# Kernel tuning notes

Hardware: AMD Instinct MI355X
Metric: run time of the kernel (lower is better)

Reference implementation:

```python
import math
import jax, jax.numpy as jnp
import numpy as np

BATCH, SEQ, EMBED, HEADS = 2, 2048, 1024, 16
HEAD_DIM = EMBED // HEADS


def setup_inputs() -> dict:
    key = jax.random.key(0)
    k1, k2, k3 = jax.random.split(key, 3)
    scale = 1.0 / math.sqrt(EMBED)  # keep pre-softmax logits in a sane range
    x = jax.random.normal(k1, (BATCH, SEQ, EMBED), dtype=jnp.float32)
    mask = jnp.ones((BATCH, SEQ), dtype=jnp.int32)
    qkv_w = jax.random.normal(k2, (3 * EMBED, EMBED), dtype=jnp.float32) * scale
    out_w = jax.random.normal(k3, (EMBED, EMBED), dtype=jnp.float32) * scale
    out_b = jnp.zeros((EMBED,), dtype=jnp.float32)
    return {"x": x, "mask": mask, "qkv_w": qkv_w, "out_w": out_w, "out_b": out_b}


def reference(x, mask, qkv_w, out_w, out_b):
    b, s, e = x.shape
    # qkv projection (torch Linear: x @ W.T), then split heads
    qkv = (x @ qkv_w.T).reshape(b, s, 3, HEADS, HEAD_DIM)
    q, k, v = qkv[:, :, 0], qkv[:, :, 1], qkv[:, :, 2]  # each [b,s,h,d]
    # full score matrix [b,h,s,s]
    scores = jnp.einsum('bshd,bthd->bhst', q, k) / math.sqrt(HEAD_DIM)
    # mask broadcast over query dim and heads: [b,1,1,s_keys]
    scores = jnp.where(mask[:, None, None, :] == 0, -jnp.inf, scores)
    attn = jax.nn.softmax(scores, axis=-1)
    # dropout is identity in eval mode
    out = jnp.einsum('bhst,bthd->bshd', attn, v).reshape(b, s, e)
    return out @ out_w.T + out_b
```

## Files before the change

kernel.cpp:

```cpp
#include <hip/hip_runtime.h>
#include <hip/hip_bf16.h>

#define BATCH 2
#define SEQ   2048
#define EMBED 1024
#define HEADS 16
#define HDIM  64
#define NBH   (BATCH*HEADS)

typedef __attribute__((ext_vector_type(8))) short short8;
typedef __attribute__((ext_vector_type(4))) float floatx4;
typedef unsigned short u16;
typedef unsigned int   u32;

__device__ __forceinline__ void async_cp16(const void* g, void* l) {
  __builtin_amdgcn_global_load_lds((const __attribute__((address_space(1))) void*)g,
                                   (__attribute__((address_space(3))) void*)l,
                                   16, 0, 0);
}

__device__ __forceinline__ u16 f2b(float f) {
  union { float f; u32 u; } x; x.f = f;
  return (u16)((x.u + 0x7fffu + ((x.u >> 16) & 1u)) >> 16);
}
__device__ __forceinline__ u32 pk2(float a, float b) {
  __hip_bfloat162 t = __float22bfloat162_rn(make_float2(a, b));
  return *reinterpret_cast<u32*>(&t);
}

__global__ __launch_bounds__(256)
void cvt_all(const float* __restrict__ x, const float* __restrict__ wqkv,
             const float* __restrict__ wo,
             u16* __restrict__ xb, u16* __restrict__ wqkvb, u16* __restrict__ wob) {
  const size_t t = (size_t)blockIdx.x * 256 + threadIdx.x;
  const float* src; u16* dst; size_t off;
  if (t < 1048576) { src = x; dst = xb; off = t; }
  else if (t < 1048576 + 786432) { src = wqkv; dst = wqkvb; off = t - 1048576; }
  else { src = wo; dst = wob; off = t - (1048576 + 786432); }
  float4 v = *(const float4*)(src + off * 4);
  ushort4 o;
  o.x = f2b(v.x); o.y = f2b(v.y); o.z = f2b(v.z); o.w = f2b(v.w);
  *(ushort4*)(dst + off * 4) = o;
}

__global__ __launch_bounds__(256, 2)
void qkv_gemm(const u16* __restrict__ X, const u16* __restrict__ W,
              u16* __restrict__ q_ws, u16* __restrict__ k_ws, u16* __restrict__ v_ws) {
  __shared__ u16 As[4][128][8];
  __shared__ u16 Bs[4][128][8];
  const int tid  = threadIdx.x;
  const int lane = tid & 63, wv = tid >> 6;
  const int l15  = lane & 15, quad = lane >> 4;
  const int wm = (wv >> 1) << 6, wn = (wv & 1) << 6;
  const int m0 = blockIdx.y << 7, n0 = blockIdx.x << 7;

  floatx4 acc[4][4];
#pragma unroll
  for (int i = 0; i < 4; ++i)
#pragma unroll
    for (int j = 0; j < 4; ++j) acc[i][j] = {0.f, 0.f, 0.f, 0.f};

  for (int k0 = 0; k0 < EMBED; k0 += 32) {
    __syncthreads();
#pragma unroll
    for (int i = 0; i < 2; ++i) {
      int c = tid + (i << 8);
      int kb = c >> 7, row = c & 127;
      async_cp16(X + (size_t)(m0 + row) * EMBED + k0 + kb * 8, &As[kb][row][0]);
      async_cp16(W + (size_t)(n0 + row) * EMBED + k0 + kb * 8, &Bs[kb][row][0]);
    }
    __syncthreads();

    short8 af[4], bf[4];
#pragma unroll
    for (int t = 0; t < 4; ++t) {
      af[t] = *(const short8*)&As[quad][wm + t * 16 + l15][0];
      bf[t] = *(const short8*)&Bs[quad][wn + t * 16 + l15][0];
    }
#pragma unroll
    for (int i = 0; i < 4; ++i)
#pragma unroll
      for (int j = 0; j < 4; ++j)
        acc[i][j] = __builtin_amdgcn_mfma_f32_16x16x32_bf16(af[i], bf[j], acc[i][j], 0, 0, 0);
  }

#pragma unroll
  for (int i = 0; i < 4; ++i) {
#pragma unroll
    for (int j = 0; j < 4; ++j) {
      int col = n0 + wn + j * 16 + l15;
      int c = col >> 10, hd = col & 1023;
      int h = hd >> 6, d = hd & 63;
      u16* dst = (c == 0) ? q_ws : (c == 1) ? k_ws : v_ws;
#pragma unroll
      for (int r = 0; r < 4; ++r) {
        int m = m0 + wm + i * 16 + quad * 4 + r;
        int b = m >> 11, s = m & 2047;
        dst[(((size_t)(b * HEADS + h)) * SEQ + s) * HDIM + d] = f2b(acc[i][j][r]);
      }
    }
  }
}

__global__ __launch_bounds__(256, 4)
void attn_kernel(const u16* __restrict__ q_ws, const u16* __restrict__ k_ws,
                 const u16* __restrict__ v_ws, const int* __restrict__ mask,
                 u16* __restrict__ ao) {
  __shared__ u16 Ks[8][64][8];
  __shared__ u16 Vt[64][72];
  __shared__ u16 Ps[4][16][72];
  __shared__ float msk[64];

  const int tid  = threadIdx.x;
  const int lane = tid & 63, wv = tid >> 6;
  const int l15  = lane & 15, quad = lane >> 4;
  const int bh = blockIdx.y;
  const int b  = bh >> 4, h = bh & 15;
  const int qrw = (blockIdx.x << 6) + (wv << 4);

  const u16* Qb = q_ws + (size_t)bh * SEQ * HDIM;
  const u16* Kb = k_ws + (size_t)bh * SEQ * HDIM;
  const u16* Vb = v_ws + (size_t)bh * SEQ * HDIM;

  short8 qf[2];
#pragma unroll
  for (int s = 0; s < 2; ++s) {
    short8 v = *(const short8*)(Qb + (size_t)(qrw + l15) * HDIM + s * 32 + quad * 8);
#pragma unroll
    for (int e = 0; e < 8; ++e) {
      union { float f; u32 u; } x;
      x.u = ((u32)(u16)v[e]) << 16;
      x.f *= 0.125f;
      v[e] = (short)(x.u >> 16);
    }
    qf[s] = v;
  }

  float m_run = -1e30f, l_run = 0.f;
  floatx4 O[4];
#pragma unroll
  for (int dt = 0; dt < 4; ++dt) O[dt] = {0.f, 0.f, 0.f, 0.f};

  const int p = tid >> 3, d0 = (tid & 7) * 8;
  short8 vr0 = *(const short8*)(Vb + (size_t)(2 * p) * HDIM + d0);
  short8 vr1 = *(const short8*)(Vb + (size_t)(2 * p + 1) * HDIM + d0);

  for (int t0 = 0; t0 < SEQ; t0 += 64) {
    __syncthreads();
#pragma unroll
    for (int i = 0; i < 2; ++i) {
      int c = tid + (i << 8);
      int kb = c >> 6, t = c & 63;
      async_cp16(Kb + (size_t)(t0 + t) * HDIM + kb * 8, &Ks[kb][t][0]);
    }
#pragma unroll
    for (int j = 0; j < 8; ++j) {
      u32 pk = ((u32)(u16)vr0[j]) | (((u32)(u16)vr1[j]) << 16);
      *(u32*)&Vt[d0 + j][2 * p] = pk;
    }
    if (tid < 64) msk[tid] = mask[b * SEQ + t0 + tid] ? 0.f : -1e30f;
    __syncthreads();

    if (t0 + 64 < SEQ) {
      vr0 = *(const short8*)(Vb + (size_t)(t0 + 64 + 2 * p) * HDIM + d0);
      vr1 = *(const short8*)(Vb + (size_t)(t0 + 64 + 2 * p + 1) * HDIM + d0);
    }

    floatx4 sc[4];
#pragma unroll
    for (int nt = 0; nt < 4; ++nt) {
      sc[nt] = {0.f, 0.f, 0.f, 0.f};
#pragma unroll
      for (int s = 0; s < 2; ++s) {
        short8 kf = *(const short8*)&Ks[s * 4 + quad][nt * 16 + l15][0];
        sc[nt] = __builtin_amdgcn_mfma_f32_16x16x32_bf16(kf, qf[s], sc[nt], 0, 0, 0);
      }
    }

    float mt = -1e30f;
#pragma unroll
    for (int nt = 0; nt < 4; ++nt) {
      const float4 m4 = *(const float4*)&msk[nt * 16 + quad * 4];
#pragma unroll
      for (int r = 0; r < 4; ++r) {
        sc[nt][r] += (&m4.x)[r];
        mt = fmaxf(mt, sc[nt][r]);
      }
    }
    mt = fmaxf(mt, __shfl_xor(mt, 16));
    mt = fmaxf(mt, __shfl_xor(mt, 32));

    const float mn = fmaxf(m_run, mt);
    const float al = __expf(m_run - mn);
    m_run = mn;

    float rs = 0.f;
#pragma unroll
    for (int nt = 0; nt < 4; ++nt) {
      float pv[4];
#pragma unroll
      for (int r = 0; r < 4; ++r) { pv[r] = __expf(sc[nt][r] - mn); rs += pv[r]; }
      uint2 w;
      w.x = pk2(pv[0], pv[1]); w.y = pk2(pv[2], pv[3]);
      *(uint2*)&Ps[wv][l15][nt * 16 + (quad << 2)] = w;
    }
    rs += __shfl_xor(rs, 16);
    rs += __shfl_xor(rs, 32);
    l_run = l_run * al + rs;

#pragma unroll
    for (int dt = 0; dt < 4; ++dt)
#pragma unroll
      for (int r = 0; r < 4; ++r) O[dt][r] *= al;

#pragma unroll
    for (int tch = 0; tch < 2; ++tch) {
      short8 pf = *(const short8*)&Ps[wv][l15][tch * 32 + quad * 8];
#pragma unroll
      for (int dt = 0; dt < 4; ++dt) {
        short8 vf = *(const short8*)&Vt[dt * 16 + l15][tch * 32 + quad * 8];
        O[dt] = __builtin_amdgcn_mfma_f32_16x16x32_bf16(vf, pf, O[dt], 0, 0, 0);
      }
    }
  }

  const float inv = 1.f / l_run;
  const size_t rowbase = ((size_t)(b * SEQ + qrw + l15)) * EMBED + h * 64;
#pragma unroll
  for (int dt = 0; dt < 4; ++dt) {
    uint2 w;
    w.x = pk2(O[dt][0] * inv, O[dt][1] * inv);
    w.y = pk2(O[dt][2] * inv, O[dt][3] * inv);
    *(uint2*)(ao + rowbase + dt * 16 + (quad << 2)) = w;
  }
}

__global__ __launch_bounds__(256, 2)
void proj_gemm(const u16* __restrict__ A, const u16* __restrict__ W,
               const float* __restrict__ bias, float* __restrict__ out) {
  __shared__ u16 As[4][128][8];
  __shared__ u16 Bs[4][64][8];
  const int tid  = threadIdx.x;
  const int lane = tid & 63, wv = tid >> 6;
  const int l15  = lane & 15, quad = lane >> 4;
  const int wm = (wv >> 1) << 6, wn = (wv & 1) << 5;
  const int m0 = blockIdx.y << 7, n0 = blockIdx.x << 6;

  floatx4 acc[4][2];
#pragma unroll
  for (int i = 0; i < 4; ++i)
#pragma unroll
    for (int j = 0; j < 2; ++j) acc[i][j] = {0.f, 0.f, 0.f, 0.f};

  for (int k0 = 0; k0 < EMBED; k0 += 32) {
    __syncthreads();
#pragma unroll
    for (int i = 0; i < 2; ++i) {
      int c = tid + (i << 8);
      int kb = c >> 7, row = c & 127;
      async_cp16(A + (size_t)(m0 + row) * EMBED + k0 + kb * 8, &As[kb][row][0]);
    }
    {
      int kb = tid >> 6, row = tid & 63;
      async_cp16(W + (size_t)(n0 + row) * EMBED + k0 + kb * 8, &Bs[kb][row][0]);
    }
    __syncthreads();

    short8 af[4], bf[2];
#pragma unroll
    for (int t = 0; t < 4; ++t)
      af[t] = *(const short8*)&As[quad][wm + t * 16 + l15][0];
#pragma unroll
    for (int t = 0; t < 2; ++t)
      bf[t] = *(const short8*)&Bs[quad][wn + t * 16 + l15][0];
#pragma unroll
    for (int i = 0; i < 4; ++i)
#pragma unroll
      for (int j = 0; j < 2; ++j)
        acc[i][j] = __builtin_amdgcn_mfma_f32_16x16x32_bf16(af[i], bf[j], acc[i][j], 0, 0, 0);
  }

#pragma unroll
  for (int i = 0; i < 4; ++i) {
#pragma unroll
    for (int j = 0; j < 2; ++j) {
      int col = n0 + wn + j * 16 + l15;
      float bv = bias[col];
#pragma unroll
      for (int r = 0; r < 4; ++r) {
        int m = m0 + wm + i * 16 + quad * 4 + r;
        out[(size_t)m * EMBED + col] = acc[i][j][r] + bv;
      }
    }
  }
}

extern "C" void kernel_launch(void* const* d_in, const int* in_sizes, int n_in,
                              void* d_out, int out_size, void* d_ws, size_t ws_size,
                              hipStream_t stream) {
  const float* x     = (const float*)d_in[0];
  const int*   mask  = (const int*)d_in[1];
  const float* qkv_w = (const float*)d_in[2];
  const float* out_w = (const float*)d_in[3];
  const float* out_b = (const float*)d_in[4];
  float* out = (float*)d_out;

  const size_t per = (size_t)NBH * SEQ * HDIM;
  u16* xb    = (u16*)d_ws;
  u16* wqkvb = xb + 4194304;
  u16* wob   = wqkvb + 3145728;
  u16* q_ws  = wob + 1048576;
  u16* k_ws  = q_ws + per;
  u16* v_ws  = k_ws + per;
  u16* ao    = v_ws + per;

  cvt_all<<<8192, 256, 0, stream>>>(x, qkv_w, out_w, xb, wqkvb, wob);
  qkv_gemm<<<dim3(24, 32), 256, 0, stream>>>(xb, wqkvb, q_ws, k_ws, v_ws);
  attn_kernel<<<dim3(SEQ / 64, NBH), 256, 0, stream>>>(q_ws, k_ws, v_ws, mask, ao);
  proj_gemm<<<dim3(16, 32), 256, 0, stream>>>(ao, wob, out_b, out);
}
```

Measured before the change: 263.0 us.

## Emit V transposed from GEMM and vectorize GEMM epilogue stores

Splits the QKV GEMM into a Q/K GEMM and a separate V GEMM. The V GEMM writes V in a transposed [bh][d][s] layout, so the attention kernel can async-copy V tiles straight into LDS instead of transposing them in registers each iteration. The Q/K and output-projection GEMMs swap MFMA operand order so each lane holds four consecutive columns, which allows packed 8-byte bf16 stores and float4 output stores in place of scalar strided writes. This adds one more kernel launch and drops the register prefetch of the next V tile, which could expose global load latency in attention.

```diff
diff --git a/kernel.cpp b/kernel.cpp
--- a/kernel.cpp
+++ b/kernel.cpp
@@ -44,8 +44,8 @@
 }
 
 __global__ __launch_bounds__(256, 2)
-void qkv_gemm(const u16* __restrict__ X, const u16* __restrict__ W,
-              u16* __restrict__ q_ws, u16* __restrict__ k_ws, u16* __restrict__ v_ws) {
+void qk_gemm(const u16* __restrict__ X, const u16* __restrict__ W,
+             u16* __restrict__ q_ws, u16* __restrict__ k_ws) {
   __shared__ u16 As[4][128][8];
   __shared__ u16 Bs[4][128][8];
   const int tid  = threadIdx.x;
@@ -81,34 +81,93 @@
     for (int i = 0; i < 4; ++i)
 #pragma unroll
       for (int j = 0; j < 4; ++j)
+        acc[i][j] = __builtin_amdgcn_mfma_f32_16x16x32_bf16(bf[j], af[i], acc[i][j], 0, 0, 0);
+  }
+
+  const int m = m0 + wm ;
+#pragma unroll
+  for (int i = 0; i < 4; ++i) {
+    int mg = m + i * 16 + l15;
+    int b = mg >> 11, s = mg & 2047;
+#pragma unroll
+    for (int j = 0; j < 4; ++j) {
+      int col0 = n0 + wn + j * 16 + (quad << 2);
+      int c = col0 >> 10, hd = col0 & 1023;
+      int h = hd >> 6, d0 = hd & 63;
+      u16* dst = c ? k_ws : q_ws;
+      uint2 w;
+      w.x = pk2(acc[i][j][0], acc[i][j][1]);
+      w.y = pk2(acc[i][j][2], acc[i][j][3]);
+      *(uint2*)(dst + (((size_t)(b * HEADS + h)) * SEQ + s) * HDIM + d0) = w;
+    }
+  }
+}
+
+__global__ __launch_bounds__(256, 2)
+void v_gemm(const u16* __restrict__ X, const u16* __restrict__ W,
+            u16* __restrict__ vT_ws) {
+  __shared__ u16 As[4][128][8];
+  __shared__ u16 Bs[4][128][8];
+  const int tid  = threadIdx.x;
+  const int lane = tid & 63, wv = tid >> 6;
+  const int l15  = lane & 15, quad = lane >> 4;
+  const int wm = (wv >> 1) << 6, wn = (wv & 1) << 6;
+  const int m0 = blockIdx.y << 7, n0 = 2048 + (blockIdx.x << 7);
+
+  floatx4 acc[4][4];
+#pragma unroll
+  for (int i = 0; i < 4; ++i)
+#pragma unroll
+    for (int j = 0; j < 4; ++j) acc[i][j] = {0.f, 0.f, 0.f, 0.f};
+
+  for (int k0 = 0; k0 < EMBED; k0 += 32) {
+    __syncthreads();
+#pragma unroll
+    for (int i = 0; i < 2; ++i) {
+      int c = tid + (i << 8);
+      int kb = c >> 7, row = c & 127;
+      async_cp16(X + (size_t)(m0 + row) * EMBED + k0 + kb * 8, &As[kb][row][0]);
+      async_cp16(W + (size_t)(n0 + row) * EMBED + k0 + kb * 8, &Bs[kb][row][0]);
+    }
+    __syncthreads();
+
+    short8 af[4], bf[4];
+#pragma unroll
+    for (int t = 0; t < 4; ++t) {
+      af[t] = *(const short8*)&As[quad][wm + t * 16 + l15][0];
+      bf[t] = *(const short8*)&Bs[quad][wn + t * 16 + l15][0];
+    }
+#pragma unroll
+    for (int i = 0; i < 4; ++i)
+#pragma unroll
+      for (int j = 0; j < 4; ++j)
         acc[i][j] = __builtin_amdgcn_mfma_f32_16x16x32_bf16(af[i], bf[j], acc[i][j], 0, 0, 0);
   }
 
 #pragma unroll
   for (int i = 0; i < 4; ++i) {
+    int mg0 = m0 + wm + i * 16 + (quad << 2);
+    int b = mg0 >> 11, s0 = mg0 & 2047;
 #pragma unroll
     for (int j = 0; j < 4; ++j) {
       int col = n0 + wn + j * 16 + l15;
-      int c = col >> 10, hd = col & 1023;
+      int hd = col & 1023;
       int h = hd >> 6, d = hd & 63;
-      u16* dst = (c == 0) ? q_ws : (c == 1) ? k_ws : v_ws;
-#pragma unroll
-      for (int r = 0; r < 4; ++r) {
-        int m = m0 + wm + i * 16 + quad * 4 + r;
-        int b = m >> 11, s = m & 2047;
-        dst[(((size_t)(b * HEADS + h)) * SEQ + s) * HDIM + d] = f2b(acc[i][j][r]);
-      }
+      uint2 w;
+      w.x = pk2(acc[i][j][0], acc[i][j][1]);
+      w.y = pk2(acc[i][j][2], acc[i][j][3]);
+      *(uint2*)(vT_ws + (((size_t)(b * HEADS + h)) * HDIM + d) * SEQ + s0) = w;
     }
   }
 }
 
 __global__ __launch_bounds__(256, 4)
 void attn_kernel(const u16* __restrict__ q_ws, const u16* __restrict__ k_ws,
-                 const u16* __restrict__ v_ws, const int* __restrict__ mask,
+                 const u16* __restrict__ vT_ws, const int* __restrict__ mask,
                  u16* __restrict__ ao) {
   __shared__ u16 Ks[8][64][8];
-  __shared__ u16 Vt[64][72];
-  __shared__ u16 Ps[4][16][72];
+  __shared__ u16 Vt[8][64][8];
+  __shared__ u16 Ps[4][16][68];
   __shared__ float msk[64];
 
   const int tid  = threadIdx.x;
@@ -118,9 +177,9 @@
   const int b  = bh >> 4, h = bh & 15;
   const int qrw = (blockIdx.x << 6) + (wv << 4);
 
-  const u16* Qb = q_ws + (size_t)bh * SEQ * HDIM;
-  const u16* Kb = k_ws + (size_t)bh * SEQ * HDIM;
-  const u16* Vb = v_ws + (size_t)bh * SEQ * HDIM;
+  const u16* Qb  = q_ws  + (size_t)bh * SEQ * HDIM;
+  const u16* Kb  = k_ws  + (size_t)bh * SEQ * HDIM;
+  const u16* VbT = vT_ws + (size_t)bh * HDIM * SEQ;
 
   short8 qf[2];
 #pragma unroll
@@ -141,30 +200,17 @@
 #pragma unroll
   for (int dt = 0; dt < 4; ++dt) O[dt] = {0.f, 0.f, 0.f, 0.f};
 
-  const int p = tid >> 3, d0 = (tid & 7) * 8;
-  short8 vr0 = *(const short8*)(Vb + (size_t)(2 * p) * HDIM + d0);
-  short8 vr1 = *(const short8*)(Vb + (size_t)(2 * p + 1) * HDIM + d0);
-
   for (int t0 = 0; t0 < SEQ; t0 += 64) {
     __syncthreads();
 #pragma unroll
     for (int i = 0; i < 2; ++i) {
       int c = tid + (i << 8);
-      int kb = c >> 6, t = c & 63;
-      async_cp16(Kb + (size_t)(t0 + t) * HDIM + kb * 8, &Ks[kb][t][0]);
-    }
-#pragma unroll
-    for (int j = 0; j < 8; ++j) {
-      u32 pk = ((u32)(u16)vr0[j]) | (((u32)(u16)vr1[j]) << 16);
-      *(u32*)&Vt[d0 + j][2 * p] = pk;
+      int kb = c >> 6, r = c & 63;
+      async_cp16(Kb + (size_t)(t0 + r) * HDIM + kb * 8, &Ks[kb][r][0]);
+      async_cp16(VbT + (size_t)r * SEQ + t0 + kb * 8, &Vt[kb][r][0]);
     }
     if (tid < 64) msk[tid] = mask[b * SEQ + t0 + tid] ? 0.f : -1e30f;
     __syncthreads();
-
-    if (t0 + 64 < SEQ) {
-      vr0 = *(const short8*)(Vb + (size_t)(t0 + 64 + 2 * p) * HDIM + d0);
-      vr1 = *(const short8*)(Vb + (size_t)(t0 + 64 + 2 * p + 1) * HDIM + d0);
-    }
 
     floatx4 sc[4];
 #pragma unroll
@@ -218,7 +264,7 @@
       short8 pf = *(const short8*)&Ps[wv][l15][tch * 32 + quad * 8];
 #pragma unroll
       for (int dt = 0; dt < 4; ++dt) {
-        short8 vf = *(const short8*)&Vt[dt * 16 + l15][tch * 32 + quad * 8];
+        short8 vf = *(const short8*)&Vt[tch * 4 + quad][dt * 16 + l15][0];
         O[dt] = __builtin_amdgcn_mfma_f32_16x16x32_bf16(vf, pf, O[dt], 0, 0, 0);
       }
     }
@@ -277,20 +323,22 @@
     for (int i = 0; i < 4; ++i)
 #pragma unroll
       for (int j = 0; j < 2; ++j)
-        acc[i][j] = __builtin_amdgcn_mfma_f32_16x16x32_bf16(af[i], bf[j], acc[i][j], 0, 0, 0);
+        acc[i][j] = __builtin_amdgcn_mfma_f32_16x16x32_bf16(bf[j], af[i], acc[i][j], 0, 0, 0);
   }
 
 #pragma unroll
   for (int i = 0; i < 4; ++i) {
+    int m = m0 + wm + i * 16 + l15;
 #pragma unroll
     for (int j = 0; j < 2; ++j) {
-      int col = n0 + wn + j * 16 + l15;
-      float bv = bias[col];
-#pragma unroll
-      for (int r = 0; r < 4; ++r) {
-        int m = m0 + wm + i * 16 + quad * 4 + r;
-        out[(size_t)m * EMBED + col] = acc[i][j][r] + bv;
-      }
+      int col0 = n0 + wn + j * 16 + (quad << 2);
+      float4 bv = *(const float4*)(bias + col0);
+      float4 o;
+      o.x = acc[i][j][0] + bv.x;
+      o.y = acc[i][j][1] + bv.y;
+      o.z = acc[i][j][2] + bv.z;
+      o.w = acc[i][j][3] + bv.w;
+      *(float4*)(out + (size_t)m * EMBED + col0) = o;
     }
   }
 }
@@ -311,11 +359,12 @@
   u16* wob   = wqkvb + 3145728;
   u16* q_ws  = wob + 1048576;
   u16* k_ws  = q_ws + per;
-  u16* v_ws  = k_ws + per;
-  u16* ao    = v_ws + per;
+  u16* vT_ws = k_ws + per;
+  u16* ao    = vT_ws + per;
 
   cvt_all<<<8192, 256, 0, stream>>>(x, qkv_w, out_w, xb, wqkvb, wob);
-  qkv_gemm<<<dim3(24, 32), 256, 0, stream>>>(xb, wqkvb, q_ws, k_ws, v_ws);
-  attn_kernel<<<dim3(SEQ / 64, NBH), 256, 0, stream>>>(q_ws, k_ws, v_ws, mask, ao);
+  qk_gemm<<<dim3(16, 32), 256, 0, stream>>>(xb, wqkvb, q_ws, k_ws);
+  v_gemm<<<dim3(8, 32), 256, 0, stream>>>(xb, wqkvb, vT_ws);
+  attn_kernel<<<dim3(SEQ / 64, NBH), 256, 0, stream>>>(q_ws, k_ws, vT_ws, mask, ao);
   proj_gemm<<<dim3(16, 32), 256, 0, stream>>>(ao, wob, out_b, out);
 }
```

New measurement: 261.5 us. Within noise of the previous version (-0.6%).
